# Optimization experiments

Measured on AMD Instinct MI355X. Metric: run time of the kernel, lower is better.

## Reference

```python
import jax, jax.numpy as jnp
import numpy as np

B, S, D = 4, 2048, 512
H = 8
DK = D // H
DFF = 2048
EPS = 1e-5


def _layernorm(x, g, b):
    mu = jnp.mean(x, axis=-1, keepdims=True)
    var = jnp.mean((x - mu) ** 2, axis=-1, keepdims=True)
    return (x - mu) * jax.lax.rsqrt(var + EPS) * g + b


def setup_inputs() -> dict:
    key = jax.random.key(0)
    ks = jax.random.split(key, 12)
    s = 1.0 / np.sqrt(D)
    sf = 1.0 / np.sqrt(DFF)
    return {
        "x": jax.random.normal(ks[0], (B, S, D), dtype=jnp.float32),
        "Wq": jax.random.uniform(ks[1], (D, D), jnp.float32, -s, s),
        "bq": jnp.zeros((D,), jnp.float32),
        "Wk": jax.random.uniform(ks[2], (D, D), jnp.float32, -s, s),
        "bk": jnp.zeros((D,), jnp.float32),
        "Wv": jax.random.uniform(ks[3], (D, D), jnp.float32, -s, s),
        "bv": jnp.zeros((D,), jnp.float32),
        "Wo": jax.random.uniform(ks[4], (D, D), jnp.float32, -s, s),
        "bo": jnp.zeros((D,), jnp.float32),
        "W1": jax.random.uniform(ks[5], (D, DFF), jnp.float32, -s, s),
        "b1": jnp.zeros((DFF,), jnp.float32),
        "W2": jax.random.uniform(ks[6], (DFF, D), jnp.float32, -sf, sf),
        "b2": jnp.zeros((D,), jnp.float32),
        "g1": jnp.ones((D,), jnp.float32),
        "be1": jnp.zeros((D,), jnp.float32),
        "g2": jnp.ones((D,), jnp.float32),
        "be2": jnp.zeros((D,), jnp.float32),
    }


def reference(x, Wq, bq, Wk, bk, Wv, bv, Wo, bo, W1, b1, W2, b2, g1, be1, g2, be2):
    # Multi-head attention (dropout = identity at eval)
    def heads(v):  # [B,S,D] -> [B,H,S,DK]
        return v.reshape(B, S, H, DK).transpose(0, 2, 1, 3)

    q = heads(x @ Wq + bq)
    k = heads(x @ Wk + bk)
    v = heads(x @ Wv + bv)
    scores = jnp.einsum("bhsd,bhtd->bhst", q, k) / np.sqrt(DK)
    attn = jax.nn.softmax(scores, axis=-1)
    ctx = jnp.einsum("bhst,bhtd->bhsd", attn, v)
    ctx = ctx.transpose(0, 2, 1, 3).reshape(B, S, D)
    attn_out = ctx @ Wo + bo

    x1 = _layernorm(x + attn_out, g1, be1)

    ff = jax.nn.relu(x1 @ W1 + b1) @ W2 + b2
    return _layernorm(x1 + ff, g2, be2)
```

## Files before the change

### kernel.cpp

```cpp
#include <hip/hip_runtime.h>
#include <hip/hip_bf16.h>
#include <stdint.h>

typedef __bf16 bf16;
typedef __attribute__((ext_vector_type(8))) __bf16 bf16x8;
typedef __attribute__((ext_vector_type(4))) float f32x4;

#define DEVI __device__ __forceinline__

constexpr int Bz = 4, Sz = 2048, Dz = 512, Hz = 8, DKz = 64, DFFz = 2048;
constexpr int ROWSz = Bz * Sz;
constexpr float EPSf = 1e-5f;
constexpr float C2f = 0.125f * 1.44269504088896f;

DEVI void load_lds16(void* lds, const void* g) {
  __builtin_amdgcn_global_load_lds(
      (const __attribute__((address_space(1))) void*)(uintptr_t)(g),
      (__attribute__((address_space(3))) void*)(uint32_t)(uintptr_t)(lds),
      16, 0, 0);
}

template <int BM, int EPI>
__global__ __launch_bounds__(256) void gemm_bt(
    const bf16* __restrict__ A, const bf16* __restrict__ Bt,
    const float* __restrict__ bias, const float* __restrict__ resid,
    void* __restrict__ Cout, int M, int N, int K) {
  constexpr int BN = 128, BK = 64;
  constexpr int MI = BM / 32;
  __shared__ alignas(16) bf16 sA[BM * BK];
  __shared__ alignas(16) bf16 sB[BN * BK];
  const int tid = threadIdx.x;
  const int lane = tid & 63;
  const int wv = tid >> 6;
  const int n0 = blockIdx.x * BN;
  const int m0 = blockIdx.y * BM;

  const int srow = lane >> 3;
  const int sch = ((lane & 7) ^ srow) * 8;
  const bf16* gA = A + (size_t)(m0 + wv * (BM / 4) + srow) * K + sch;
  const bf16* gB = Bt + (size_t)(n0 + wv * 32 + srow) * K + sch;

  const int wm = (wv >> 1) * (BM / 2);
  const int wn = (wv & 1) * 64;
  const int fr = lane & 15;
  const int fq = lane >> 4;

  f32x4 acc[MI][4] = {};

  for (int k0 = 0; k0 < K; k0 += BK) {
#pragma unroll
    for (int j = 0; j < BM / 32; ++j)
      load_lds16(sA + (wv * (BM / 4) + j * 8) * BK, gA + (size_t)(j * 8) * K + k0);
#pragma unroll
    for (int j = 0; j < 4; ++j)
      load_lds16(sB + (wv * 32 + j * 8) * BK, gB + (size_t)(j * 8) * K + k0);
    __syncthreads();
#pragma unroll
    for (int kk = 0; kk < 2; ++kk) {
      const int fc = ((4 * kk + fq) ^ (fr & 7)) * 8;
      bf16x8 af[MI], bfr[4];
#pragma unroll
      for (int i = 0; i < MI; ++i)
        af[i] = *(const bf16x8*)(sA + (wm + i * 16 + fr) * BK + fc);
#pragma unroll
      for (int j = 0; j < 4; ++j)
        bfr[j] = *(const bf16x8*)(sB + (wn + j * 16 + fr) * BK + fc);
#pragma unroll
      for (int i = 0; i < MI; ++i)
#pragma unroll
        for (int j = 0; j < 4; ++j)
          acc[i][j] = __builtin_amdgcn_mfma_f32_16x16x32_bf16(af[i], bfr[j], acc[i][j], 0, 0, 0);
    }
    __syncthreads();
  }

#pragma unroll
  for (int i = 0; i < MI; ++i) {
#pragma unroll
    for (int j = 0; j < 4; ++j) {
      const int col = n0 + wn + j * 16 + fr;
      const float bv = bias[col];
#pragma unroll
      for (int r = 0; r < 4; ++r) {
        const int row = m0 + wm + i * 16 + fq * 4 + r;
        const size_t idx = (size_t)row * N + col;
        float v = acc[i][j][r] + bv;
        if (EPI == 0) {
          ((bf16*)Cout)[idx] = (bf16)v;
        } else if (EPI == 1) {
          ((float*)Cout)[idx] = v + resid[idx];
        } else if (EPI == 2) {
          ((bf16*)Cout)[idx] = (bf16)(v > 0.f ? v : 0.f);
        } else {
          ((bf16*)Cout)[idx] = (bf16)(col < 512 ? v * C2f : v);
        }
      }
    }
  }
}

__global__ __launch_bounds__(256, 2) void flash_attn(
    const bf16* __restrict__ qkv, const bf16* __restrict__ Vt,
    bf16* __restrict__ ctx) {
  const int bid = blockIdx.x;
  const int qt = bid & 15;
  const int h = (bid >> 4) & 7;
  const int b = bid >> 7;
  const int q0 = qt * 128;
  const int tid = threadIdx.x, lane = tid & 63, wv = tid >> 6;
  const int fr = lane & 15, fq = lane >> 4;
  const int xsw = fr & 7;

  __shared__ alignas(16) bf16 sK[2][64 * 64];
  __shared__ alignas(16) bf16 sV[2][64 * 64];
  __shared__ alignas(16) bf16 sP[128 * 64];

  const int srow = lane >> 3;
  const int scol = ((lane & 7) ^ srow) * 8;

  const bf16* gQ = qkv + (size_t)(b * Sz + q0 + wv * 32 + srow) * 1536 + h * 64 + scol;
  const bf16* gK = qkv + (size_t)(b * Sz + wv * 16 + srow) * 1536 + 512 + h * 64 + scol;
  const bf16* gV = Vt + (size_t)((b * 8 + h) * 64 + wv * 16 + srow) * Sz + scol;

#pragma unroll
  for (int i = 0; i < 4; ++i)
    load_lds16(sP + (wv * 32 + i * 8) * 64, gQ + (size_t)(i * 8) * 1536);
  load_lds16(sK[0] + (wv * 16 + 0) * 64, gK);
  load_lds16(sK[0] + (wv * 16 + 8) * 64, gK + (size_t)8 * 1536);
  load_lds16(sV[0] + (wv * 16 + 0) * 64, gV);
  load_lds16(sV[0] + (wv * 16 + 8) * 64, gV + (size_t)8 * Sz);
  asm volatile("s_waitcnt vmcnt(0)" ::: "memory");
  __syncthreads();

  const int colc0 = (fq ^ xsw) * 8;
  const int colc1 = ((fq + 4) ^ xsw) * 8;
  int pcol[4], qsrc[4];
#pragma unroll
  for (int j = 0; j < 4; ++j)
    pcol[j] = (((fq + 4 * j) >> 1) ^ xsw) * 8 + (fq & 1) * 4;
#pragma unroll
  for (int r = 0; r < 4; ++r) qsrc[r] = (fq * 4 + r) | (lane & 48);

  bf16x8 qb[2][2];
#pragma unroll
  for (int s = 0; s < 2; ++s) {
    qb[s][0] = *(const bf16x8*)(sP + (wv * 32 + s * 16 + fr) * 64 + colc0);
    qb[s][1] = *(const bf16x8*)(sP + (wv * 32 + s * 16 + fr) * 64 + colc1);
  }
  asm volatile("s_waitcnt lgkmcnt(0)" ::: "memory");

  float l_part[2] = {0.f, 0.f};
  f32x4 acc_o[2][4] = {};

  for (int it = 0; it < 32; ++it) {
    const int cur = it & 1;
    if (it + 1 < 32) {
      const int nxt = cur ^ 1;
      const size_t t1 = (size_t)(it + 1) * 64;
      load_lds16(sK[nxt] + (wv * 16 + 0) * 64, gK + t1 * 1536);
      load_lds16(sK[nxt] + (wv * 16 + 8) * 64, gK + (t1 + 8) * 1536);
      load_lds16(sV[nxt] + (wv * 16 + 0) * 64, gV + t1);
      load_lds16(sV[nxt] + (wv * 16 + 8) * 64, gV + (size_t)8 * Sz + t1);
    }

    bf16x8 kf[2][4];
#pragma unroll
    for (int j = 0; j < 4; ++j) {
      kf[0][j] = *(const bf16x8*)(sK[cur] + (j * 16 + fr) * 64 + colc0);
      kf[1][j] = *(const bf16x8*)(sK[cur] + (j * 16 + fr) * 64 + colc1);
    }
    f32x4 sc[2][4] = {};
#pragma unroll
    for (int s = 0; s < 2; ++s)
#pragma unroll
      for (int kk = 0; kk < 2; ++kk)
#pragma unroll
        for (int j = 0; j < 4; ++j)
          sc[s][j] = __builtin_amdgcn_mfma_f32_16x16x32_bf16(kf[kk][j], qb[s][kk], sc[s][j], 0, 0, 0);

#pragma unroll
    for (int s = 0; s < 2; ++s) {
      float rs = 0.f;
#pragma unroll
      for (int j = 0; j < 4; ++j) {
        float e0 = __builtin_amdgcn_exp2f(sc[s][j][0]);
        float e1 = __builtin_amdgcn_exp2f(sc[s][j][1]);
        float e2 = __builtin_amdgcn_exp2f(sc[s][j][2]);
        float e3 = __builtin_amdgcn_exp2f(sc[s][j][3]);
        rs += (e0 + e1) + (e2 + e3);
        bf16 pt[4] = {(bf16)e0, (bf16)e1, (bf16)e2, (bf16)e3};
        *(uint2*)(sP + (wv * 32 + s * 16 + fr) * 64 + pcol[j]) = *(const uint2*)pt;
      }
      l_part[s] += rs;
    }
    asm volatile("s_waitcnt lgkmcnt(0)" ::: "memory");

    bf16x8 vf[2][4];
#pragma unroll
    for (int j = 0; j < 4; ++j) {
      vf[0][j] = *(const bf16x8*)(sV[cur] + (j * 16 + fr) * 64 + colc0);
      vf[1][j] = *(const bf16x8*)(sV[cur] + (j * 16 + fr) * 64 + colc1);
    }
#pragma unroll
    for (int s = 0; s < 2; ++s)
#pragma unroll
      for (int kk = 0; kk < 2; ++kk) {
        bf16x8 ap = *(const bf16x8*)(sP + (wv * 32 + s * 16 + fr) * 64 + (kk ? colc1 : colc0));
#pragma unroll
        for (int j = 0; j < 4; ++j)
          acc_o[s][j] = __builtin_amdgcn_mfma_f32_16x16x32_bf16(ap, vf[kk][j], acc_o[s][j], 0, 0, 0);
      }
    __syncthreads();
  }

#pragma unroll
  for (int s = 0; s < 2; ++s) {
    float l = l_part[s];
    l += __shfl_xor(l, 16, 64);
    l += __shfl_xor(l, 32, 64);
    float rl[4];
#pragma unroll
    for (int r = 0; r < 4; ++r) rl[r] = 1.0f / __shfl(l, qsrc[r], 64);
#pragma unroll
    for (int j = 0; j < 4; ++j)
#pragma unroll
      for (int r = 0; r < 4; ++r) {
        const int row = b * Sz + q0 + wv * 32 + s * 16 + fq * 4 + r;
        const int col = h * 64 + j * 16 + fr;
        ctx[(size_t)row * Dz + col] = (bf16)(acc_o[s][j][r] * rl[r]);
      }
  }
}

template <int WRITE_BF>
__global__ __launch_bounds__(256) void layer_norm_k(
    const float* __restrict__ y, const float* __restrict__ g,
    const float* __restrict__ be, float* __restrict__ outf,
    bf16* __restrict__ outb) {
  const int row = blockIdx.x * 4 + (threadIdx.x >> 6);
  const int lane = threadIdx.x & 63;
  const float4* yr = (const float4*)(y + (size_t)row * Dz);
  float4 v0 = yr[lane * 2];
  float4 v1 = yr[lane * 2 + 1];
  float s = v0.x + v0.y + v0.z + v0.w + v1.x + v1.y + v1.z + v1.w;
  float ss = v0.x * v0.x + v0.y * v0.y + v0.z * v0.z + v0.w * v0.w +
             v1.x * v1.x + v1.y * v1.y + v1.z * v1.z + v1.w * v1.w;
#pragma unroll
  for (int o = 1; o < 64; o <<= 1) {
    s += __shfl_xor(s, o, 64);
    ss += __shfl_xor(ss, o, 64);
  }
  const float mu = s * (1.0f / Dz);
  const float rstd = rsqrtf(ss * (1.0f / Dz) - mu * mu + EPSf);
  const int col = lane * 8;
  const float4* g4 = (const float4*)(g + col);
  const float4* b4 = (const float4*)(be + col);
  float4 ga = g4[0], gb = g4[1], ba = b4[0], bb = b4[1];
  float4 o0, o1;
  o0.x = (v0.x - mu) * rstd * ga.x + ba.x;
  o0.y = (v0.y - mu) * rstd * ga.y + ba.y;
  o0.z = (v0.z - mu) * rstd * ga.z + ba.z;
  o0.w = (v0.w - mu) * rstd * ga.w + ba.w;
  o1.x = (v1.x - mu) * rstd * gb.x + bb.x;
  o1.y = (v1.y - mu) * rstd * gb.y + bb.y;
  o1.z = (v1.z - mu) * rstd * gb.z + bb.z;
  o1.w = (v1.w - mu) * rstd * gb.w + bb.w;
  float4* of = (float4*)(outf + (size_t)row * Dz + col);
  of[0] = o0;
  of[1] = o1;
  if (WRITE_BF) {
    bf16 ob[8] = {(bf16)o0.x, (bf16)o0.y, (bf16)o0.z, (bf16)o0.w,
                  (bf16)o1.x, (bf16)o1.y, (bf16)o1.z, (bf16)o1.w};
    *(uint4*)(outb + (size_t)row * Dz + col) = *(const uint4*)ob;
  }
}

__global__ __launch_bounds__(256) void prep_all(
    const float* __restrict__ Wq, const float* __restrict__ Wk,
    const float* __restrict__ Wv, const float* __restrict__ Wo,
    const float* __restrict__ W1, const float* __restrict__ W2,
    const float* __restrict__ bq, const float* __restrict__ bk,
    const float* __restrict__ bv, const float* __restrict__ x,
    bf16* __restrict__ WqkvT, bf16* __restrict__ WoT,
    bf16* __restrict__ W1T, bf16* __restrict__ W2T,
    float* __restrict__ bqkv, bf16* __restrict__ xb) {
  __shared__ float tile[64][65];
  const int blk = blockIdx.x;
  const int t = threadIdx.x;
  if (blk < 768) {
    const float* W;
    bf16* Wt;
    int K, N, local;
    if (blk < 64)       { W = Wq; Wt = WqkvT;                       K = 512;  N = 512;  local = blk; }
    else if (blk < 128) { W = Wk; Wt = WqkvT + (size_t)512 * 512;   K = 512;  N = 512;  local = blk - 64; }
    else if (blk < 192) { W = Wv; Wt = WqkvT + (size_t)1024 * 512;  K = 512;  N = 512;  local = blk - 128; }
    else if (blk < 256) { W = Wo; Wt = WoT;                         K = 512;  N = 512;  local = blk - 192; }
    else if (blk < 512) { W = W1; Wt = W1T;                         K = 512;  N = 2048; local = blk - 256; }
    else                { W = W2; Wt = W2T;                         K = 2048; N = 512;  local = blk - 512; }
    const int kt = K / 64;
    const int k0 = (local % kt) * 64, n0 = (local / kt) * 64;
    const int r = t >> 2, c = (t & 3) * 16;
    const float* src = W + (size_t)(k0 + r) * N + n0 + c;
#pragma unroll
    for (int i = 0; i < 4; ++i) {
      float4 v = ((const float4*)src)[i];
      tile[r][c + i * 4 + 0] = v.x;
      tile[r][c + i * 4 + 1] = v.y;
      tile[r][c + i * 4 + 2] = v.z;
      tile[r][c + i * 4 + 3] = v.w;
    }
    __syncthreads();
    union { bf16 hh[16]; uint4 u[2]; } pk;
#pragma unroll
    for (int i = 0; i < 16; ++i) pk.hh[i] = (bf16)tile[c + i][r];
    uint4* dst = (uint4*)(Wt + (size_t)(n0 + r) * K + k0 + c);
    dst[0] = pk.u[0];
    dst[1] = pk.u[1];
  } else if (blk == 768) {
    for (int i = t; i < 1536; i += 256)
      bqkv[i] = i < 512 ? bq[i] : (i < 1024 ? bk[i - 512] : bv[i - 1024]);
  } else {
    const int local = blk - 769;
#pragma unroll
    for (int k = 0; k < 4; ++k) {
      const int i = local * 1024 + k * 256 + t;
      float4 v = ((const float4*)x)[i];
      bf16 tv[4] = {(bf16)v.x, (bf16)v.y, (bf16)v.z, (bf16)v.w};
      ((uint2*)xb)[i] = *(const uint2*)tv;
    }
  }
}

__global__ __launch_bounds__(256) void vtrans(
    const bf16* __restrict__ qkv, bf16* __restrict__ Vt) {
  __shared__ bf16 tile[64][65];
  const int bh = blockIdx.x, s0 = blockIdx.y * 64;
  const int b = bh >> 3, h = bh & 7;
  const int t = threadIdx.x, r = t >> 2, c = (t & 3) * 16;
  const bf16* src = qkv + (size_t)(b * Sz + s0 + r) * 1536 + 1024 + h * 64 + c;
  bf16 tmp[16];
  *(uint4*)&tmp[0] = ((const uint4*)src)[0];
  *(uint4*)&tmp[8] = ((const uint4*)src)[1];
#pragma unroll
  for (int i = 0; i < 16; ++i) tile[r][c + i] = tmp[i];
  __syncthreads();
  union { bf16 hh[16]; uint4 u[2]; } pk;
#pragma unroll
  for (int i = 0; i < 16; ++i) pk.hh[i] = tile[c + i][r];
  uint4* dst = (uint4*)(Vt + (size_t)(bh * 64 + r) * Sz + s0 + c);
  dst[0] = pk.u[0];
  dst[1] = pk.u[1];
}

extern "C" void kernel_launch(void* const* d_in, const int* in_sizes, int n_in,
                              void* d_out, int out_size, void* d_ws, size_t ws_size,
                              hipStream_t stream) {
  const float* x   = (const float*)d_in[0];
  const float* Wq  = (const float*)d_in[1];
  const float* bq  = (const float*)d_in[2];
  const float* Wk  = (const float*)d_in[3];
  const float* bk  = (const float*)d_in[4];
  const float* Wv  = (const float*)d_in[5];
  const float* bvp = (const float*)d_in[6];
  const float* Wo  = (const float*)d_in[7];
  const float* bo  = (const float*)d_in[8];
  const float* W1  = (const float*)d_in[9];
  const float* b1  = (const float*)d_in[10];
  const float* W2  = (const float*)d_in[11];
  const float* b2  = (const float*)d_in[12];
  const float* g1  = (const float*)d_in[13];
  const float* be1 = (const float*)d_in[14];
  const float* g2  = (const float*)d_in[15];
  const float* be2 = (const float*)d_in[16];

  char* ws = (char*)d_ws;
  size_t off = 0;
  auto alloc = [&](size_t bytes) -> void* {
    void* p = ws + off;
    off += (bytes + 255) & ~(size_t)255;
    return p;
  };
  bf16*  WqkvT = (bf16*)alloc((size_t)1536 * 512 * 2);
  float* bqkv  = (float*)alloc(1536 * 4);
  bf16*  WoT   = (bf16*)alloc((size_t)512 * 512 * 2);
  bf16*  W1T   = (bf16*)alloc((size_t)2048 * 512 * 2);
  bf16*  W2T   = (bf16*)alloc((size_t)512 * 2048 * 2);
  bf16*  xb    = (bf16*)alloc((size_t)ROWSz * 512 * 2);
  bf16*  qkv   = (bf16*)alloc((size_t)ROWSz * 1536 * 2);
  bf16*  Vt    = (bf16*)alloc((size_t)32 * 64 * 2048 * 2);
  bf16*  ctx   = (bf16*)alloc((size_t)ROWSz * 512 * 2);
  float* y1    = (float*)alloc((size_t)ROWSz * 512 * 4);
  float* x1f   = (float*)alloc((size_t)ROWSz * 512 * 4);
  bf16*  x1b   = (bf16*)alloc((size_t)ROWSz * 512 * 2);
  bf16*  hbuf  = qkv;
  float* y2    = y1;

  prep_all<<<dim3(1793), 256, 0, stream>>>(Wq, Wk, Wv, Wo, W1, W2, bq, bk, bvp, x,
                                           WqkvT, WoT, W1T, W2T, bqkv, xb);

  gemm_bt<128, 3><<<dim3(12, 64), 256, 0, stream>>>(xb, WqkvT, bqkv, nullptr, qkv, ROWSz, 1536, 512);
  vtrans<<<dim3(32, 32), 256, 0, stream>>>(qkv, Vt);
  flash_attn<<<dim3(512), 256, 0, stream>>>(qkv, Vt, ctx);
  gemm_bt<64, 1><<<dim3(4, 128), 256, 0, stream>>>(ctx, WoT, bo, x, y1, ROWSz, 512, 512);
  layer_norm_k<1><<<dim3(2048), 256, 0, stream>>>(y1, g1, be1, x1f, x1b);
  gemm_bt<128, 2><<<dim3(16, 64), 256, 0, stream>>>(x1b, W1T, b1, nullptr, hbuf, ROWSz, 2048, 512);
  gemm_bt<64, 1><<<dim3(4, 128), 256, 0, stream>>>(hbuf, W2T, b2, x1f, y2, ROWSz, 512, 2048);
  layer_norm_k<0><<<dim3(2048), 256, 0, stream>>>(y2, g2, be2, (float*)d_out, nullptr);
}
```

Baseline: 269.2 us.

## Double-buffer GEMM LDS, widen attention KV stages, and store residual intermediates in bf16

The GEMM k-loop now uses double-buffered LDS tiles so the next K tile is prefetched while the current one is multiplied. Flash attention stages 128 keys per pipeline step, two 64-key halves, which halves the number of barriers. The residual-add outputs and the first layernorm result are stored as bf16 instead of fp32, and the second residual reads the bf16 x1, cutting global traffic. In exchange LDS use rises, which may lower occupancy, and the bf16 intermediates add rounding error.

```diff
diff --git a/kernel.cpp b/kernel.cpp
--- a/kernel.cpp
+++ b/kernel.cpp
@@ -24,11 +24,12 @@
 __global__ __launch_bounds__(256) void gemm_bt(
     const bf16* __restrict__ A, const bf16* __restrict__ Bt,
     const float* __restrict__ bias, const float* __restrict__ resid,
+    const bf16* __restrict__ residb,
     void* __restrict__ Cout, int M, int N, int K) {
   constexpr int BN = 128, BK = 64;
   constexpr int MI = BM / 32;
-  __shared__ alignas(16) bf16 sA[BM * BK];
-  __shared__ alignas(16) bf16 sB[BN * BK];
+  __shared__ alignas(16) bf16 sA[2][BM * BK];
+  __shared__ alignas(16) bf16 sB[2][BN * BK];
   const int tid = threadIdx.x;
   const int lane = tid & 63;
   const int wv = tid >> 6;
@@ -45,26 +46,34 @@
   const int fr = lane & 15;
   const int fq = lane >> 4;
 
+  auto stage = [&](int buf, int k0) {
+#pragma unroll
+    for (int j = 0; j < BM / 32; ++j)
+      load_lds16(sA[buf] + (wv * (BM / 4) + j * 8) * BK, gA + (size_t)(j * 8) * K + k0);
+#pragma unroll
+    for (int j = 0; j < 4; ++j)
+      load_lds16(sB[buf] + (wv * 32 + j * 8) * BK, gB + (size_t)(j * 8) * K + k0);
+  };
+
   f32x4 acc[MI][4] = {};
 
-  for (int k0 = 0; k0 < K; k0 += BK) {
-#pragma unroll
-    for (int j = 0; j < BM / 32; ++j)
-      load_lds16(sA + (wv * (BM / 4) + j * 8) * BK, gA + (size_t)(j * 8) * K + k0);
-#pragma unroll
-    for (int j = 0; j < 4; ++j)
-      load_lds16(sB + (wv * 32 + j * 8) * BK, gB + (size_t)(j * 8) * K + k0);
-    __syncthreads();
+  stage(0, 0);
+  __syncthreads();
+
+  const int niter = K / BK;
+  for (int it = 0; it < niter; ++it) {
+    const int cur = it & 1;
+    if (it + 1 < niter) stage(cur ^ 1, (it + 1) * BK);
 #pragma unroll
     for (int kk = 0; kk < 2; ++kk) {
       const int fc = ((4 * kk + fq) ^ (fr & 7)) * 8;
       bf16x8 af[MI], bfr[4];
 #pragma unroll
       for (int i = 0; i < MI; ++i)
-        af[i] = *(const bf16x8*)(sA + (wm + i * 16 + fr) * BK + fc);
+        af[i] = *(const bf16x8*)(sA[cur] + (wm + i * 16 + fr) * BK + fc);
 #pragma unroll
       for (int j = 0; j < 4; ++j)
-        bfr[j] = *(const bf16x8*)(sB + (wn + j * 16 + fr) * BK + fc);
+        bfr[j] = *(const bf16x8*)(sB[cur] + (wn + j * 16 + fr) * BK + fc);
 #pragma unroll
       for (int i = 0; i < MI; ++i)
 #pragma unroll
@@ -85,14 +94,14 @@
         const int row = m0 + wm + i * 16 + fq * 4 + r;
         const size_t idx = (size_t)row * N + col;
         float v = acc[i][j][r] + bv;
-        if (EPI == 0) {
-          ((bf16*)Cout)[idx] = (bf16)v;
-        } else if (EPI == 1) {
-          ((float*)Cout)[idx] = v + resid[idx];
+        if (EPI == 1) {
+          ((bf16*)Cout)[idx] = (bf16)(v + resid[idx]);
         } else if (EPI == 2) {
           ((bf16*)Cout)[idx] = (bf16)(v > 0.f ? v : 0.f);
+        } else if (EPI == 3) {
+          ((bf16*)Cout)[idx] = (bf16)(col < 512 ? v * C2f : v);
         } else {
-          ((bf16*)Cout)[idx] = (bf16)(col < 512 ? v * C2f : v);
+          ((bf16*)Cout)[idx] = (bf16)(v + (float)residb[idx]);
         }
       }
     }
@@ -111,8 +120,8 @@
   const int fr = lane & 15, fq = lane >> 4;
   const int xsw = fr & 7;
 
-  __shared__ alignas(16) bf16 sK[2][64 * 64];
-  __shared__ alignas(16) bf16 sV[2][64 * 64];
+  __shared__ alignas(16) bf16 sK[2][2][64 * 64];
+  __shared__ alignas(16) bf16 sV[2][2][64 * 64];
   __shared__ alignas(16) bf16 sP[128 * 64];
 
   const int srow = lane >> 3;
@@ -122,13 +131,20 @@
   const bf16* gK = qkv + (size_t)(b * Sz + wv * 16 + srow) * 1536 + 512 + h * 64 + scol;
   const bf16* gV = Vt + (size_t)((b * 8 + h) * 64 + wv * 16 + srow) * Sz + scol;
 
+  auto stageKV = [&](int buf, int t0) {
+#pragma unroll
+    for (int hf = 0; hf < 2; ++hf) {
+      load_lds16(sK[buf][hf] + (wv * 16 + 0) * 64, gK + (size_t)(t0 + hf * 64) * 1536);
+      load_lds16(sK[buf][hf] + (wv * 16 + 8) * 64, gK + (size_t)(t0 + hf * 64 + 8) * 1536);
+      load_lds16(sV[buf][hf] + (wv * 16 + 0) * 64, gV + t0 + hf * 64);
+      load_lds16(sV[buf][hf] + (wv * 16 + 8) * 64, gV + (size_t)8 * Sz + t0 + hf * 64);
+    }
+  };
+
 #pragma unroll
   for (int i = 0; i < 4; ++i)
     load_lds16(sP + (wv * 32 + i * 8) * 64, gQ + (size_t)(i * 8) * 1536);
-  load_lds16(sK[0] + (wv * 16 + 0) * 64, gK);
-  load_lds16(sK[0] + (wv * 16 + 8) * 64, gK + (size_t)8 * 1536);
-  load_lds16(sV[0] + (wv * 16 + 0) * 64, gV);
-  load_lds16(sV[0] + (wv * 16 + 8) * 64, gV + (size_t)8 * Sz);
+  stageKV(0, 0);
   asm volatile("s_waitcnt vmcnt(0)" ::: "memory");
   __syncthreads();
 
@@ -152,64 +168,63 @@
   float l_part[2] = {0.f, 0.f};
   f32x4 acc_o[2][4] = {};
 
-  for (int it = 0; it < 32; ++it) {
-    const int cur = it & 1;
-    if (it + 1 < 32) {
-      const int nxt = cur ^ 1;
-      const size_t t1 = (size_t)(it + 1) * 64;
-      load_lds16(sK[nxt] + (wv * 16 + 0) * 64, gK + t1 * 1536);
-      load_lds16(sK[nxt] + (wv * 16 + 8) * 64, gK + (t1 + 8) * 1536);
-      load_lds16(sV[nxt] + (wv * 16 + 0) * 64, gV + t1);
-      load_lds16(sV[nxt] + (wv * 16 + 8) * 64, gV + (size_t)8 * Sz + t1);
-    }
-
-    bf16x8 kf[2][4];
-#pragma unroll
-    for (int j = 0; j < 4; ++j) {
-      kf[0][j] = *(const bf16x8*)(sK[cur] + (j * 16 + fr) * 64 + colc0);
-      kf[1][j] = *(const bf16x8*)(sK[cur] + (j * 16 + fr) * 64 + colc1);
-    }
-    f32x4 sc[2][4] = {};
-#pragma unroll
-    for (int s = 0; s < 2; ++s)
-#pragma unroll
-      for (int kk = 0; kk < 2; ++kk)
-#pragma unroll
-        for (int j = 0; j < 4; ++j)
-          sc[s][j] = __builtin_amdgcn_mfma_f32_16x16x32_bf16(kf[kk][j], qb[s][kk], sc[s][j], 0, 0, 0);
-
-#pragma unroll
-    for (int s = 0; s < 2; ++s) {
-      float rs = 0.f;
+  for (int ot = 0; ot < 16; ++ot) {
+    const int cur = ot & 1;
+    if (ot + 1 < 16) stageKV(cur ^ 1, (ot + 1) * 128);
+
+#pragma unroll
+    for (int hf = 0; hf < 2; ++hf) {
+      const bf16* sKc = sK[cur][hf];
+      const bf16* sVc = sV[cur][hf];
+
+      bf16x8 kf[2][4];
 #pragma unroll
       for (int j = 0; j < 4; ++j) {
-        float e0 = __builtin_amdgcn_exp2f(sc[s][j][0]);
-        float e1 = __builtin_amdgcn_exp2f(sc[s][j][1]);
-        float e2 = __builtin_amdgcn_exp2f(sc[s][j][2]);
-        float e3 = __builtin_amdgcn_exp2f(sc[s][j][3]);
-        rs += (e0 + e1) + (e2 + e3);
-        bf16 pt[4] = {(bf16)e0, (bf16)e1, (bf16)e2, (bf16)e3};
-        *(uint2*)(sP + (wv * 32 + s * 16 + fr) * 64 + pcol[j]) = *(const uint2*)pt;
+        kf[0][j] = *(const bf16x8*)(sKc + (j * 16 + fr) * 64 + colc0);
+        kf[1][j] = *(const bf16x8*)(sKc + (j * 16 + fr) * 64 + colc1);
       }
-      l_part[s] += rs;
-    }
-    asm volatile("s_waitcnt lgkmcnt(0)" ::: "memory");
-
-    bf16x8 vf[2][4];
-#pragma unroll
-    for (int j = 0; j < 4; ++j) {
-      vf[0][j] = *(const bf16x8*)(sV[cur] + (j * 16 + fr) * 64 + colc0);
-      vf[1][j] = *(const bf16x8*)(sV[cur] + (j * 16 + fr) * 64 + colc1);
-    }
-#pragma unroll
-    for (int s = 0; s < 2; ++s)
-#pragma unroll
-      for (int kk = 0; kk < 2; ++kk) {
-        bf16x8 ap = *(const bf16x8*)(sP + (wv * 32 + s * 16 + fr) * 64 + (kk ? colc1 : colc0));
-#pragma unroll
-        for (int j = 0; j < 4; ++j)
-          acc_o[s][j] = __builtin_amdgcn_mfma_f32_16x16x32_bf16(ap, vf[kk][j], acc_o[s][j], 0, 0, 0);
+      f32x4 sc[2][4] = {};
+#pragma unroll
+      for (int s = 0; s < 2; ++s)
+#pragma unroll
+        for (int kk = 0; kk < 2; ++kk)
+#pragma unroll
+          for (int j = 0; j < 4; ++j)
+            sc[s][j] = __builtin_amdgcn_mfma_f32_16x16x32_bf16(kf[kk][j], qb[s][kk], sc[s][j], 0, 0, 0);
+
+#pragma unroll
+      for (int s = 0; s < 2; ++s) {
+        float rs = 0.f;
+#pragma unroll
+        for (int j = 0; j < 4; ++j) {
+          float e0 = __builtin_amdgcn_exp2f(sc[s][j][0]);
+          float e1 = __builtin_amdgcn_exp2f(sc[s][j][1]);
+          float e2 = __builtin_amdgcn_exp2f(sc[s][j][2]);
+          float e3 = __builtin_amdgcn_exp2f(sc[s][j][3]);
+          rs += (e0 + e1) + (e2 + e3);
+          bf16 pt[4] = {(bf16)e0, (bf16)e1, (bf16)e2, (bf16)e3};
+          *(uint2*)(sP + (wv * 32 + s * 16 + fr) * 64 + pcol[j]) = *(const uint2*)pt;
+        }
+        l_part[s] += rs;
       }
+      asm volatile("s_waitcnt lgkmcnt(0)" ::: "memory");
+
+      bf16x8 vf[2][4];
+#pragma unroll
+      for (int j = 0; j < 4; ++j) {
+        vf[0][j] = *(const bf16x8*)(sVc + (j * 16 + fr) * 64 + colc0);
+        vf[1][j] = *(const bf16x8*)(sVc + (j * 16 + fr) * 64 + colc1);
+      }
+#pragma unroll
+      for (int s = 0; s < 2; ++s)
+#pragma unroll
+        for (int kk = 0; kk < 2; ++kk) {
+          bf16x8 ap = *(const bf16x8*)(sP + (wv * 32 + s * 16 + fr) * 64 + (kk ? colc1 : colc0));
+#pragma unroll
+          for (int j = 0; j < 4; ++j)
+            acc_o[s][j] = __builtin_amdgcn_mfma_f32_16x16x32_bf16(ap, vf[kk][j], acc_o[s][j], 0, 0, 0);
+        }
+    }
     __syncthreads();
   }
 
@@ -232,19 +247,22 @@
   }
 }
 
-template <int WRITE_BF>
+template <int OUT_F32>
 __global__ __launch_bounds__(256) void layer_norm_k(
-    const float* __restrict__ y, const float* __restrict__ g,
-    const float* __restrict__ be, float* __restrict__ outf,
-    bf16* __restrict__ outb) {
+    const bf16* __restrict__ y, const float* __restrict__ g,
+    const float* __restrict__ be, void* __restrict__ out) {
   const int row = blockIdx.x * 4 + (threadIdx.x >> 6);
   const int lane = threadIdx.x & 63;
-  const float4* yr = (const float4*)(y + (size_t)row * Dz);
-  float4 v0 = yr[lane * 2];
-  float4 v1 = yr[lane * 2 + 1];
-  float s = v0.x + v0.y + v0.z + v0.w + v1.x + v1.y + v1.z + v1.w;
-  float ss = v0.x * v0.x + v0.y * v0.y + v0.z * v0.z + v0.w * v0.w +
-             v1.x * v1.x + v1.y * v1.y + v1.z * v1.z + v1.w * v1.w;
+  const int col = lane * 8;
+  bf16x8 hv = *(const bf16x8*)(y + (size_t)row * Dz + col);
+  float v[8];
+  float s = 0.f, ss = 0.f;
+#pragma unroll
+  for (int i = 0; i < 8; ++i) {
+    v[i] = (float)hv[i];
+    s += v[i];
+    ss += v[i] * v[i];
+  }
 #pragma unroll
   for (int o = 1; o < 64; o <<= 1) {
     s += __shfl_xor(s, o, 64);
@@ -252,26 +270,27 @@
   }
   const float mu = s * (1.0f / Dz);
   const float rstd = rsqrtf(ss * (1.0f / Dz) - mu * mu + EPSf);
-  const int col = lane * 8;
   const float4* g4 = (const float4*)(g + col);
   const float4* b4 = (const float4*)(be + col);
   float4 ga = g4[0], gb = g4[1], ba = b4[0], bb = b4[1];
-  float4 o0, o1;
-  o0.x = (v0.x - mu) * rstd * ga.x + ba.x;
-  o0.y = (v0.y - mu) * rstd * ga.y + ba.y;
-  o0.z = (v0.z - mu) * rstd * ga.z + ba.z;
-  o0.w = (v0.w - mu) * rstd * ga.w + ba.w;
-  o1.x = (v1.x - mu) * rstd * gb.x + bb.x;
-  o1.y = (v1.y - mu) * rstd * gb.y + bb.y;
-  o1.z = (v1.z - mu) * rstd * gb.z + bb.z;
-  o1.w = (v1.w - mu) * rstd * gb.w + bb.w;
-  float4* of = (float4*)(outf + (size_t)row * Dz + col);
-  of[0] = o0;
-  of[1] = o1;
-  if (WRITE_BF) {
-    bf16 ob[8] = {(bf16)o0.x, (bf16)o0.y, (bf16)o0.z, (bf16)o0.w,
-                  (bf16)o1.x, (bf16)o1.y, (bf16)o1.z, (bf16)o1.w};
-    *(uint4*)(outb + (size_t)row * Dz + col) = *(const uint4*)ob;
+  float o8[8];
+  o8[0] = (v[0] - mu) * rstd * ga.x + ba.x;
+  o8[1] = (v[1] - mu) * rstd * ga.y + ba.y;
+  o8[2] = (v[2] - mu) * rstd * ga.z + ba.z;
+  o8[3] = (v[3] - mu) * rstd * ga.w + ba.w;
+  o8[4] = (v[4] - mu) * rstd * gb.x + bb.x;
+  o8[5] = (v[5] - mu) * rstd * gb.y + bb.y;
+  o8[6] = (v[6] - mu) * rstd * gb.z + bb.z;
+  o8[7] = (v[7] - mu) * rstd * gb.w + bb.w;
+  if (OUT_F32) {
+    float4* of = (float4*)((float*)out + (size_t)row * Dz + col);
+    of[0] = make_float4(o8[0], o8[1], o8[2], o8[3]);
+    of[1] = make_float4(o8[4], o8[5], o8[6], o8[7]);
+  } else {
+    bf16 ob[8];
+#pragma unroll
+    for (int i = 0; i < 8; ++i) ob[i] = (bf16)o8[i];
+    *(uint4*)((bf16*)out + (size_t)row * Dz + col) = *(const uint4*)ob;
   }
 }
 
@@ -389,21 +408,20 @@
   bf16*  qkv   = (bf16*)alloc((size_t)ROWSz * 1536 * 2);
   bf16*  Vt    = (bf16*)alloc((size_t)32 * 64 * 2048 * 2);
   bf16*  ctx   = (bf16*)alloc((size_t)ROWSz * 512 * 2);
-  float* y1    = (float*)alloc((size_t)ROWSz * 512 * 4);
-  float* x1f   = (float*)alloc((size_t)ROWSz * 512 * 4);
+  bf16*  y1    = (bf16*)alloc((size_t)ROWSz * 512 * 2);
   bf16*  x1b   = (bf16*)alloc((size_t)ROWSz * 512 * 2);
   bf16*  hbuf  = qkv;
-  float* y2    = y1;
+  bf16*  y2    = y1;
 
   prep_all<<<dim3(1793), 256, 0, stream>>>(Wq, Wk, Wv, Wo, W1, W2, bq, bk, bvp, x,
                                            WqkvT, WoT, W1T, W2T, bqkv, xb);
 
-  gemm_bt<128, 3><<<dim3(12, 64), 256, 0, stream>>>(xb, WqkvT, bqkv, nullptr, qkv, ROWSz, 1536, 512);
+  gemm_bt<128, 3><<<dim3(12, 64), 256, 0, stream>>>(xb, WqkvT, bqkv, nullptr, nullptr, qkv, ROWSz, 1536, 512);
   vtrans<<<dim3(32, 32), 256, 0, stream>>>(qkv, Vt);
   flash_attn<<<dim3(512), 256, 0, stream>>>(qkv, Vt, ctx);
-  gemm_bt<64, 1><<<dim3(4, 128), 256, 0, stream>>>(ctx, WoT, bo, x, y1, ROWSz, 512, 512);
-  layer_norm_k<1><<<dim3(2048), 256, 0, stream>>>(y1, g1, be1, x1f, x1b);
-  gemm_bt<128, 2><<<dim3(16, 64), 256, 0, stream>>>(x1b, W1T, b1, nullptr, hbuf, ROWSz, 2048, 512);
-  gemm_bt<64, 1><<<dim3(4, 128), 256, 0, stream>>>(hbuf, W2T, b2, x1f, y2, ROWSz, 512, 2048);
-  layer_norm_k<0><<<dim3(2048), 256, 0, stream>>>(y2, g2, be2, (float*)d_out, nullptr);
-}
+  gemm_bt<64, 1><<<dim3(4, 128), 256, 0, stream>>>(ctx, WoT, bo, x, nullptr, y1, ROWSz, 512, 512);
+  layer_norm_k<0><<<dim3(2048), 256, 0, stream>>>(y1, g1, be1, x1b);
+  gemm_bt<128, 2><<<dim3(16, 64), 256, 0, stream>>>(x1b, W1T, b1, nullptr, nullptr, hbuf, ROWSz, 2048, 512);
+  gemm_bt<64, 4><<<dim3(4, 128), 256, 0, stream>>>(hbuf, W2T, b2, nullptr, x1b, y2, ROWSz, 512, 2048);
+  layer_norm_k<1><<<dim3(2048), 256, 0, stream>>>(y2, g2, be2, d_out);
+}
```

After: 255.6 us. 1.05x faster.
